# Kernel optimization log

Hardware: AMD Instinct MI355X
Metric: run time of the kernel (lower is better)

## Reference

```python
import jax, jax.numpy as jnp
import numpy as np

NUM_HEADS = 8


def setup_inputs() -> dict:
    key = jax.random.key(0)
    ks = jax.random.split(key, 5)
    b, c, h, w = 8, 256, 32, 32
    x = jax.random.normal(ks[0], (b, c, h, w), dtype=jnp.float32)
    w_qkv = jax.random.normal(ks[1], (3 * c, c), dtype=jnp.float32) * (c ** -0.5)
    b_qkv = jax.random.normal(ks[2], (3 * c,), dtype=jnp.float32) * 0.02
    w_proj = jax.random.normal(ks[3], (c, c), dtype=jnp.float32) * (c ** -0.5)
    b_proj = jax.random.normal(ks[4], (c,), dtype=jnp.float32) * 0.02
    return {"x": x, "w_qkv": w_qkv, "b_qkv": b_qkv, "w_proj": w_proj, "b_proj": b_proj}


def reference(x, w_qkv, b_qkv, w_proj, b_proj):
    b, c, h, w = x.shape
    nh = NUM_HEADS
    dh = c // nh
    L = h * w
    scale = dh ** -0.5
    # 1x1 conv == per-pixel GEMM
    qkv = jnp.einsum('bchw,oc->bohw', x, w_qkv) + b_qkv[None, :, None, None]
    qkv = qkv.reshape(b, 3, nh, dh, L)
    q, k, v = qkv[:, 0], qkv[:, 1], qkv[:, 2]  # each (b, nh, dh, L)
    attn = jnp.einsum('bhdi,bhdj->bhij', q, k) * scale  # (b, nh, L, L)
    attn = jax.nn.softmax(attn, axis=-1)
    out = jnp.einsum('bhdj,bhij->bhdi', v, attn)  # (b, nh, dh, L)
    out = out.reshape(b, c, h, w)
    proj = jnp.einsum('bchw,oc->bohw', out, w_proj) + b_proj[None, :, None, None]
    return x + proj
```

## Files before the change

kernel.cpp:

```cpp
#include <hip/hip_runtime.h>
#include <math.h>

#define B_   8
#define CIN  256
#define L_   1024
#define NH_  8
#define DH_  32

typedef __attribute__((ext_vector_type(8))) short short8;
typedef __attribute__((ext_vector_type(4))) short short4v;
typedef __attribute__((ext_vector_type(4))) float f32x4;
typedef __attribute__((ext_vector_type(4))) unsigned int uint4v;
typedef __attribute__((ext_vector_type(2))) unsigned int uint2v;

__device__ inline short f2bf_hu(float f) {
    union { float f; unsigned u; } v; v.f = f;
    return (short)((v.u + 0x8000u) >> 16);
}
__device__ inline unsigned pkbf2(float a, float b) {
    union { float f; unsigned u; } x, y; x.f = a; y.f = b;
    return __builtin_amdgcn_perm(y.u + 0x8000u, x.u + 0x8000u, 0x07060302u);
}

__global__ __launch_bounds__(256) void qkv_gemm(
    const float* __restrict__ x, const float* __restrict__ w,
    const float* __restrict__ bias, short* __restrict__ qkvT)
{
    __shared__ short Xs[64][40];
    __shared__ short Wt[128][40];
    const int t = threadIdx.x, lane = t & 63, wv = t >> 6;
    const int n = lane & 15, quad = lane >> 4;
    const int b = blockIdx.z, o0 = blockIdx.y * 128, l0 = blockIdx.x * 64;

    float bias_r[8];
    #pragma unroll
    for (int nf = 0; nf < 8; nf++) bias_r[nf] = bias[o0 + nf * 16 + n];

    f32x4 acc[8];
    #pragma unroll
    for (int nf = 0; nf < 8; nf++) acc[nf] = (f32x4){0.f, 0.f, 0.f, 0.f};

    const int cS = t >> 3, lsS = (t & 7) * 8;

    for (int c0 = 0; c0 < CIN; c0 += 32) {
        {
            const float* xp = &x[(((size_t)b * CIN + c0 + cS) << 10) + l0 + lsS];
            const float4 xa = *(const float4*)xp;
            const float4 xb = *(const float4*)(xp + 4);
            const float vals[8] = {xa.x, xa.y, xa.z, xa.w, xb.x, xb.y, xb.z, xb.w};
            #pragma unroll
            for (int k = 0; k < 8; k++) {
                const int l = lsS + k;
                const int col = (((cS >> 3) ^ (l & 3)) << 3) | (cS & 7);
                Xs[l][col] = f2bf_hu(vals[k]);
            }
        }
        {
            const int o = t >> 1, cs = (t & 1) * 16;
            const float* wp = &w[(size_t)(o0 + o) * CIN + c0 + cs];
            const float4 w0 = *(const float4*)(wp);
            const float4 w1 = *(const float4*)(wp + 4);
            const float4 w2 = *(const float4*)(wp + 8);
            const float4 w3 = *(const float4*)(wp + 12);
            uint4v pa = { pkbf2(w0.x, w0.y), pkbf2(w0.z, w0.w),
                          pkbf2(w1.x, w1.y), pkbf2(w1.z, w1.w) };
            uint4v pb = { pkbf2(w2.x, w2.y), pkbf2(w2.z, w2.w),
                          pkbf2(w3.x, w3.y), pkbf2(w3.z, w3.w) };
            *(uint4v*)&Wt[o][cs]     = pa;
            *(uint4v*)&Wt[o][cs + 8] = pb;
        }
        __syncthreads();

        const int arow = wv * 16 + n;
        const short8 af = *(const short8*)&Xs[arow][(quad ^ (arow & 3)) * 8];
        #pragma unroll
        for (int nf = 0; nf < 8; nf++) {
            const short8 bf = *(const short8*)&Wt[nf * 16 + n][quad * 8];
            acc[nf] = __builtin_amdgcn_mfma_f32_16x16x32_bf16(af, bf, acc[nf], 0, 0, 0);
        }
        __syncthreads();
    }

    #pragma unroll
    for (int reg = 0; reg < 4; reg++) {
        const size_t l = l0 + wv * 16 + quad * 4 + reg;
        short* row = qkvT + (((size_t)b << 10) + l) * 768 + o0 + n;
        #pragma unroll
        for (int nf = 0; nf < 8; nf++)
            row[nf * 16] = f2bf_hu(acc[nf][reg] + bias_r[nf]);
    }
}

__global__ __launch_bounds__(256) void proj_gemm(
    const short* __restrict__ aT, const float* __restrict__ w,
    const float* __restrict__ bias, const float* __restrict__ resid,
    float* __restrict__ out)
{
    __shared__ short Xs[64][40];
    __shared__ short Wt[64][40];
    const int t = threadIdx.x, lane = t & 63, wv = t >> 6;
    const int n = lane & 15, quad = lane >> 4;
    const int b = blockIdx.z, o0 = blockIdx.y * 64, l0 = blockIdx.x * 64;

    float bias_r[4];
    #pragma unroll
    for (int reg = 0; reg < 4; reg++) bias_r[reg] = bias[o0 + wv * 16 + quad * 4 + reg];

    f32x4 acc[4];
    #pragma unroll
    for (int nf = 0; nf < 4; nf++) acc[nf] = (f32x4){0.f, 0.f, 0.f, 0.f};

    for (int c0 = 0; c0 < CIN; c0 += 32) {
        {
            const int l = t >> 2, cs = (t & 3) * 8;
            *(uint4v*)&Xs[l][cs] =
                *(const uint4v*)&aT[(((size_t)b << 10) + l0 + l) * CIN + c0 + cs];
        }
        {
            const int o = t >> 2, cs = (t & 3) * 8;
            const float* wp = &w[(size_t)(o0 + o) * CIN + c0 + cs];
            const float4 a4 = *(const float4*)(wp);
            const float4 b4 = *(const float4*)(wp + 4);
            uint4v pw = { pkbf2(a4.x, a4.y), pkbf2(a4.z, a4.w),
                          pkbf2(b4.x, b4.y), pkbf2(b4.z, b4.w) };
            *(uint4v*)&Wt[o][cs] = pw;
        }
        __syncthreads();

        const short8 af = *(const short8*)&Wt[wv * 16 + n][quad * 8];
        #pragma unroll
        for (int nf = 0; nf < 4; nf++) {
            const short8 bf = *(const short8*)&Xs[nf * 16 + n][quad * 8];
            acc[nf] = __builtin_amdgcn_mfma_f32_16x16x32_bf16(af, bf, acc[nf], 0, 0, 0);
        }
        __syncthreads();
    }

    #pragma unroll
    for (int reg = 0; reg < 4; reg++) {
        const int o = o0 + wv * 16 + quad * 4 + reg;
        #pragma unroll
        for (int nf = 0; nf < 4; nf++) {
            const size_t off = (((size_t)b * CIN + o) << 10) + l0 + nf * 16 + n;
            out[off] = acc[nf][reg] + bias_r[reg] + resid[off];
        }
    }
}

__global__ __launch_bounds__(256) void attn_mfma(
    const short* __restrict__ qkvT, short* __restrict__ attnoT)
{
    __shared__ short Vt[2][32][80];
    __shared__ __align__(16) char umem[128 * 88 * 2];
    short (*Ss)[88] = (short(*)[88])umem;
    float (*OtT)[38] = (float(*)[38])umem;

    const int t = threadIdx.x, lane = t & 63, wv = t >> 6;
    const int n = lane & 15, quad = lane >> 4;
    const int id = blockIdx.x;
    const int bh = id & 63;
    const int b = bh >> 3, h = bh & 7;
    const int i0 = (id >> 6) * 128;

    const short* base = qkvT + ((size_t)b << 10) * 768;

    short8 qa[2];
    #pragma unroll
    for (int a = 0; a < 2; a++)
        qa[a] = *(const short8*)&base[(size_t)(i0 + wv * 32 + a * 16 + n) * 768
                                      + h * DH_ + quad * 8];

    short8 vf2;
    {
        const short one = (n == 0) ? (short)0x3F80 : (short)0;
        #pragma unroll
        for (int u = 0; u < 8; u++) vf2[u] = one;
    }

    f32x4 o_acc[2][3];
    #pragma unroll
    for (int a = 0; a < 2; a++)
        #pragma unroll
        for (int nf = 0; nf < 3; nf++) o_acc[a][nf] = (f32x4){0.f, 0.f, 0.f, 0.f};

    const float K1 = 0.25503510f;
    const float K2 = 11.54156036f;
    const int TSTRIDE = 64 * 768;

    const short* kp0 = base + 256 + h * DH_ + (size_t)n * 768 + quad * 8;
    const short* kp1 = kp0 + 16 * 768;
    const short* kp2 = kp0 + 32 * 768;
    const short* kp3 = kp0 + 48 * 768;
    const int jS = t >> 3, dsS = (t & 7) * 4;
    const short* vp0 = base + 512 + h * DH_ + (size_t)jS * 768 + dsS;
    const short* vp1 = vp0 + 32 * 768;

    const int vmsk = ((dsS >> 2) & 7) << 3;
    const int vwo0 = dsS * 80 + (jS ^ vmsk);
    const int vwo1 = dsS * 80 + ((jS + 32) ^ vmsk);
    short* const vtb0 = &Vt[0][0][0];
    short* const vtb1 = &Vt[1][0][0];
    short* const ssw  = &Ss[wv * 32 + n][quad * 4];
    const short* const ssr = &Ss[wv * 32 + n][quad * 8];
    int vro[2][2];
    #pragma unroll
    for (int nf = 0; nf < 2; nf++) {
        const int dv = nf * 16 + n;
        const int msk = ((dv >> 2) & 7) << 3;
        #pragma unroll
        for (int kk = 0; kk < 2; kk++)
            vro[kk][nf] = dv * 80 + ((kk * 32 + quad * 8) ^ msk);
    }

    short8 kfA[4], kfB[4];

    auto stageV = [&](short* vtb) {
        const short4v a = *(const short4v*)vp0; vp0 += TSTRIDE;
        const short4v c = *(const short4v*)vp1; vp1 += TSTRIDE;
        #pragma unroll
        for (int u = 0; u < 4; u++) {
            vtb[vwo0 + u * 80] = a[u];
            vtb[vwo1 + u * 80] = c[u];
        }
    };
    auto loadK = [&](short8* kf) {
        kf[0] = *(const short8*)kp0; kp0 += TSTRIDE;
        kf[1] = *(const short8*)kp1; kp1 += TSTRIDE;
        kf[2] = *(const short8*)kp2; kp2 += TSTRIDE;
        kf[3] = *(const short8*)kp3; kp3 += TSTRIDE;
    };
    auto tile = [&](const short8* kf, const short* vtb) {
        #pragma unroll
        for (int f = 0; f < 4; f++) {
            #pragma unroll
            for (int a = 0; a < 2; a++) {
                f32x4 z = {0.f, 0.f, 0.f, 0.f};
                const f32x4 sv = __builtin_amdgcn_mfma_f32_16x16x32_bf16(kf[f], qa[a], z, 0, 0, 0);
                const float p0 = __builtin_amdgcn_exp2f(fmaf(sv[0], K1, -K2));
                const float p1 = __builtin_amdgcn_exp2f(fmaf(sv[1], K1, -K2));
                const float p2 = __builtin_amdgcn_exp2f(fmaf(sv[2], K1, -K2));
                const float p3 = __builtin_amdgcn_exp2f(fmaf(sv[3], K1, -K2));
                uint2v pk = { pkbf2(p0, p1), pkbf2(p2, p3) };
                *(uint2v*)(ssw + a * 16 * 88 + f * 16) = pk;
            }
        }
        #pragma unroll
        for (int kk = 0; kk < 2; kk++) {
            short8 pf[2];
            #pragma unroll
            for (int a = 0; a < 2; a++)
                pf[a] = *(const short8*)(ssr + a * 16 * 88 + kk * 32);
            #pragma unroll
            for (int nf = 0; nf < 2; nf++) {
                const short8 vf = *(const short8*)(vtb + vro[kk][nf]);
                #pragma unroll
                for (int a = 0; a < 2; a++)
                    o_acc[a][nf] = __builtin_amdgcn_mfma_f32_16x16x32_bf16(pf[a], vf, o_acc[a][nf], 0, 0, 0);
            }
            #pragma unroll
            for (int a = 0; a < 2; a++)
                o_acc[a][2] = __builtin_amdgcn_mfma_f32_16x16x32_bf16(pf[a], vf2, o_acc[a][2], 0, 0, 0);
        }
    };

    stageV(vtb0);
    loadK(kfA);

    for (int itp = 0; itp < 8; itp++) {
        __syncthreads();
        stageV(vtb1);
        loadK(kfB);
        tile(kfA, vtb0);
        __syncthreads();
        if (itp < 7) { stageV(vtb0); loadK(kfA); }
        tile(kfB, vtb1);
    }

    __syncthreads();
    #pragma unroll
    for (int a = 0; a < 2; a++)
        #pragma unroll
        for (int r = 0; r < 4; r++) {
            const float lv  = __shfl(o_acc[a][2][r], lane & 48, 64);
            const float inv = 1.f / lv;
            const int il = wv * 32 + a * 16 + quad * 4 + r;
            OtT[il][n]      = o_acc[a][0][r] * inv;
            OtT[il][16 + n] = o_acc[a][1][r] * inv;
        }
    __syncthreads();
    short* ob = attnoT + (((size_t)b << 10) + i0) * CIN + h * DH_;
    #pragma unroll
    for (int r = 0; r < 4; r++) {
        const int idx = t + r * 256;
        const int l = idx >> 3, cs = (idx & 7) * 4;
        uint2v pv;
        pv.x = pkbf2(OtT[l][cs],     OtT[l][cs + 1]);
        pv.y = pkbf2(OtT[l][cs + 2], OtT[l][cs + 3]);
        *(uint2v*)&ob[(size_t)l * CIN + cs] = pv;
    }
}

extern "C" void kernel_launch(void* const* d_in, const int* in_sizes, int n_in,
                              void* d_out, int out_size, void* d_ws, size_t ws_size,
                              hipStream_t stream) {
    const float* x      = (const float*)d_in[0];
    const float* w_qkv  = (const float*)d_in[1];
    const float* b_qkv  = (const float*)d_in[2];
    const float* w_proj = (const float*)d_in[3];
    const float* b_proj = (const float*)d_in[4];
    float* out = (float*)d_out;

    short* qkvT   = (short*)d_ws;
    short* attnoT = qkvT + (size_t)B_ * L_ * 768;

    qkv_gemm<<<dim3(16, 6, B_), 256, 0, stream>>>(x, w_qkv, b_qkv, qkvT);
    attn_mfma<<<dim3(512), 256, 0, stream>>>(qkvT, attnoT);
    proj_gemm<<<dim3(16, 4, B_), 256, 0, stream>>>(attnoT, w_proj, b_proj, x, out);
}
```

Before: 115.7 us.

## Store V transposed from QKV GEMM so attention reads V fragments directly from global

The QKV GEMM now writes Q and K into a token-major buffer and V into a separate channel-major (d, L) buffer. The attention kernel can then load V MFMA operands straight from global memory into registers, the same way it loads K. This removes the shared-memory V staging, its swizzled scatter writes, and both __syncthreads per iteration. In exchange, the GEMM's V epilogue does strided scalar stores, and the attention kernel relies on cache and register prefetch rather than LDS reuse for V.

```diff
diff --git a/kernel.cpp b/kernel.cpp
--- a/kernel.cpp
+++ b/kernel.cpp
@@ -24,7 +24,8 @@
 
 __global__ __launch_bounds__(256) void qkv_gemm(
     const float* __restrict__ x, const float* __restrict__ w,
-    const float* __restrict__ bias, short* __restrict__ qkvT)
+    const float* __restrict__ bias, short* __restrict__ qkT,
+    short* __restrict__ vT)
 {
     __shared__ short Xs[64][40];
     __shared__ short Wt[128][40];
@@ -81,13 +82,26 @@
         __syncthreads();
     }
 
-    #pragma unroll
-    for (int reg = 0; reg < 4; reg++) {
-        const size_t l = l0 + wv * 16 + quad * 4 + reg;
-        short* row = qkvT + (((size_t)b << 10) + l) * 768 + o0 + n;
-        #pragma unroll
-        for (int nf = 0; nf < 8; nf++)
-            row[nf * 16] = f2bf_hu(acc[nf][reg] + bias_r[nf]);
+    if (o0 < 512) {
+        #pragma unroll
+        for (int reg = 0; reg < 4; reg++) {
+            const size_t l = l0 + wv * 16 + quad * 4 + reg;
+            short* row = qkT + ((((size_t)b << 10) + l) << 9) + o0 + n;
+            #pragma unroll
+            for (int nf = 0; nf < 8; nf++)
+                row[nf * 16] = f2bf_hu(acc[nf][reg] + bias_r[nf]);
+        }
+    } else {
+        #pragma unroll
+        for (int reg = 0; reg < 4; reg++) {
+            const size_t l = l0 + wv * 16 + quad * 4 + reg;
+            #pragma unroll
+            for (int nf = 0; nf < 8; nf++) {
+                const int ov = o0 - 512 + nf * 16 + n;
+                vT[(((size_t)b << 8) + ov << 10) + l] =
+                    f2bf_hu(acc[nf][reg] + bias_r[nf]);
+            }
+        }
     }
 }
 
@@ -148,9 +162,9 @@
 }
 
 __global__ __launch_bounds__(256) void attn_mfma(
-    const short* __restrict__ qkvT, short* __restrict__ attnoT)
+    const short* __restrict__ qkT, const short* __restrict__ vT,
+    short* __restrict__ attnoT)
 {
-    __shared__ short Vt[2][32][80];
     __shared__ __align__(16) char umem[128 * 88 * 2];
     short (*Ss)[88] = (short(*)[88])umem;
     float (*OtT)[38] = (float(*)[38])umem;
@@ -162,13 +176,14 @@
     const int b = bh >> 3, h = bh & 7;
     const int i0 = (id >> 6) * 128;
 
-    const short* base = qkvT + ((size_t)b << 10) * 768;
+    const short* qbase = qkT + ((size_t)b << 19) + h * DH_;
+    const short* kbase = qbase + 256;
+    const short* vtb   = vT + ((size_t)((b << 3) + h) << 15);
 
     short8 qa[2];
     #pragma unroll
     for (int a = 0; a < 2; a++)
-        qa[a] = *(const short8*)&base[(size_t)(i0 + wv * 32 + a * 16 + n) * 768
-                                      + h * DH_ + quad * 8];
+        qa[a] = *(const short8*)&qbase[(size_t)(i0 + wv * 32 + a * 16 + n) * 512 + quad * 8];
 
     short8 vf2;
     {
@@ -185,51 +200,34 @@
 
     const float K1 = 0.25503510f;
     const float K2 = 11.54156036f;
-    const int TSTRIDE = 64 * 768;
-
-    const short* kp0 = base + 256 + h * DH_ + (size_t)n * 768 + quad * 8;
-    const short* kp1 = kp0 + 16 * 768;
-    const short* kp2 = kp0 + 32 * 768;
-    const short* kp3 = kp0 + 48 * 768;
-    const int jS = t >> 3, dsS = (t & 7) * 4;
-    const short* vp0 = base + 512 + h * DH_ + (size_t)jS * 768 + dsS;
-    const short* vp1 = vp0 + 32 * 768;
-
-    const int vmsk = ((dsS >> 2) & 7) << 3;
-    const int vwo0 = dsS * 80 + (jS ^ vmsk);
-    const int vwo1 = dsS * 80 + ((jS + 32) ^ vmsk);
-    short* const vtb0 = &Vt[0][0][0];
-    short* const vtb1 = &Vt[1][0][0];
+    const int KSTRIDE = 64 * 512;
+    const int VSTRIDE = 64;
+
+    const short* kp0 = kbase + (size_t)n * 512 + quad * 8;
+    const short* kp1 = kp0 + 16 * 512;
+    const short* kp2 = kp0 + 32 * 512;
+    const short* kp3 = kp0 + 48 * 512;
+    const short* vp00 = vtb + ((size_t)n) * 1024 + quad * 8;
+    const short* vp01 = vp00 + 16 * 1024;
+    const short* vp10 = vp00 + 32;
+    const short* vp11 = vp01 + 32;
+
     short* const ssw  = &Ss[wv * 32 + n][quad * 4];
     const short* const ssr = &Ss[wv * 32 + n][quad * 8];
-    int vro[2][2];
-    #pragma unroll
-    for (int nf = 0; nf < 2; nf++) {
-        const int dv = nf * 16 + n;
-        const int msk = ((dv >> 2) & 7) << 3;
-        #pragma unroll
-        for (int kk = 0; kk < 2; kk++)
-            vro[kk][nf] = dv * 80 + ((kk * 32 + quad * 8) ^ msk);
-    }
-
-    short8 kfA[4], kfB[4];
-
-    auto stageV = [&](short* vtb) {
-        const short4v a = *(const short4v*)vp0; vp0 += TSTRIDE;
-        const short4v c = *(const short4v*)vp1; vp1 += TSTRIDE;
-        #pragma unroll
-        for (int u = 0; u < 4; u++) {
-            vtb[vwo0 + u * 80] = a[u];
-            vtb[vwo1 + u * 80] = c[u];
-        }
+
+    short8 kfA[4], vfA[2][2], kfB[4], vfB[2][2];
+
+    auto loadKV = [&](short8* kf, short8 vf[2][2]) {
+        kf[0] = *(const short8*)kp0; kp0 += KSTRIDE;
+        kf[1] = *(const short8*)kp1; kp1 += KSTRIDE;
+        kf[2] = *(const short8*)kp2; kp2 += KSTRIDE;
+        kf[3] = *(const short8*)kp3; kp3 += KSTRIDE;
+        vf[0][0] = *(const short8*)vp00; vp00 += VSTRIDE;
+        vf[0][1] = *(const short8*)vp01; vp01 += VSTRIDE;
+        vf[1][0] = *(const short8*)vp10; vp10 += VSTRIDE;
+        vf[1][1] = *(const short8*)vp11; vp11 += VSTRIDE;
     };
-    auto loadK = [&](short8* kf) {
-        kf[0] = *(const short8*)kp0; kp0 += TSTRIDE;
-        kf[1] = *(const short8*)kp1; kp1 += TSTRIDE;
-        kf[2] = *(const short8*)kp2; kp2 += TSTRIDE;
-        kf[3] = *(const short8*)kp3; kp3 += TSTRIDE;
-    };
-    auto tile = [&](const short8* kf, const short* vtb) {
+    auto tile = [&](const short8* kf, const short8 vf[2][2]) {
         #pragma unroll
         for (int f = 0; f < 4; f++) {
             #pragma unroll
@@ -251,29 +249,22 @@
             for (int a = 0; a < 2; a++)
                 pf[a] = *(const short8*)(ssr + a * 16 * 88 + kk * 32);
             #pragma unroll
-            for (int nf = 0; nf < 2; nf++) {
-                const short8 vf = *(const short8*)(vtb + vro[kk][nf]);
+            for (int nf = 0; nf < 2; nf++)
                 #pragma unroll
                 for (int a = 0; a < 2; a++)
-                    o_acc[a][nf] = __builtin_amdgcn_mfma_f32_16x16x32_bf16(pf[a], vf, o_acc[a][nf], 0, 0, 0);
-            }
+                    o_acc[a][nf] = __builtin_amdgcn_mfma_f32_16x16x32_bf16(pf[a], vf[kk][nf], o_acc[a][nf], 0, 0, 0);
             #pragma unroll
             for (int a = 0; a < 2; a++)
                 o_acc[a][2] = __builtin_amdgcn_mfma_f32_16x16x32_bf16(pf[a], vf2, o_acc[a][2], 0, 0, 0);
         }
     };
 
-    stageV(vtb0);
-    loadK(kfA);
-
+    loadKV(kfA, vfA);
     for (int itp = 0; itp < 8; itp++) {
-        __syncthreads();
-        stageV(vtb1);
-        loadK(kfB);
-        tile(kfA, vtb0);
-        __syncthreads();
-        if (itp < 7) { stageV(vtb0); loadK(kfA); }
-        tile(kfB, vtb1);
+        loadKV(kfB, vfB);
+        tile(kfA, vfA);
+        if (itp < 7) loadKV(kfA, vfA);
+        tile(kfB, vfB);
     }
 
     __syncthreads();
@@ -310,10 +301,11 @@
     const float* b_proj = (const float*)d_in[4];
     float* out = (float*)d_out;
 
-    short* qkvT   = (short*)d_ws;
-    short* attnoT = qkvT + (size_t)B_ * L_ * 768;
-
-    qkv_gemm<<<dim3(16, 6, B_), 256, 0, stream>>>(x, w_qkv, b_qkv, qkvT);
-    attn_mfma<<<dim3(512), 256, 0, stream>>>(qkvT, attnoT);
+    short* qkT    = (short*)d_ws;
+    short* vT     = qkT + (size_t)B_ * L_ * 512;
+    short* attnoT = vT  + (size_t)B_ * CIN * L_;
+
+    qkv_gemm<<<dim3(16, 6, B_), 256, 0, stream>>>(x, w_qkv, b_qkv, qkT, vT);
+    attn_mfma<<<dim3(512), 256, 0, stream>>>(qkT, vT, attnoT);
     proj_gemm<<<dim3(16, 4, B_), 256, 0, stream>>>(attnoT, w_proj, b_proj, x, out);
 }
```

New measurement: 126.3 us. 1.09x slower.

## Retile QKV GEMM to 128x96 blocks with packed bf16 X staging

Applied to the files above, without the earlier changes.

The QKV projection GEMM moves from 64(L)x128(O) tiles to 128(L)x96(O) tiles, so each wave computes two 16-row A fragments that share every B fragment load. The X tile load is reorganised so each thread reads 4 channels x 4 pixels and writes packed bf16 pairs to shared memory, replacing 8 scalar 16-bit stores. Together these aim to cut LDS traffic and store instructions per MFMA, with the grid changing from 16x6 to 8x8 blocks per batch. In exchange, a quarter of threads sit idle during the weight load and each thread holds more accumulator registers.

```diff
diff --git a/kernel.cpp b/kernel.cpp
--- a/kernel.cpp
+++ b/kernel.cpp
@@ -26,36 +26,43 @@
     const float* __restrict__ x, const float* __restrict__ w,
     const float* __restrict__ bias, short* __restrict__ qkvT)
 {
-    __shared__ short Xs[64][40];
-    __shared__ short Wt[128][40];
+    __shared__ short Xs[128][40];
+    __shared__ short Wt[96][40];
     const int t = threadIdx.x, lane = t & 63, wv = t >> 6;
     const int n = lane & 15, quad = lane >> 4;
-    const int b = blockIdx.z, o0 = blockIdx.y * 128, l0 = blockIdx.x * 64;
-
-    float bias_r[8];
-    #pragma unroll
-    for (int nf = 0; nf < 8; nf++) bias_r[nf] = bias[o0 + nf * 16 + n];
-
-    f32x4 acc[8];
-    #pragma unroll
-    for (int nf = 0; nf < 8; nf++) acc[nf] = (f32x4){0.f, 0.f, 0.f, 0.f};
-
-    const int cS = t >> 3, lsS = (t & 7) * 8;
+    const int b = blockIdx.z, o0 = blockIdx.y * 96, l0 = blockIdx.x * 128;
+
+    float bias_r[6];
+    #pragma unroll
+    for (int nf = 0; nf < 6; nf++) bias_r[nf] = bias[o0 + nf * 16 + n];
+
+    f32x4 acc[2][6];
+    #pragma unroll
+    for (int a = 0; a < 2; a++)
+        #pragma unroll
+        for (int nf = 0; nf < 6; nf++) acc[a][nf] = (f32x4){0.f, 0.f, 0.f, 0.f};
+
+    const int cS4 = (t & 7) * 4;
+    const int lg4 = (t >> 3) * 4;
 
     for (int c0 = 0; c0 < CIN; c0 += 32) {
         {
-            const float* xp = &x[(((size_t)b * CIN + c0 + cS) << 10) + l0 + lsS];
-            const float4 xa = *(const float4*)xp;
-            const float4 xb = *(const float4*)(xp + 4);
-            const float vals[8] = {xa.x, xa.y, xa.z, xa.w, xb.x, xb.y, xb.z, xb.w};
-            #pragma unroll
-            for (int k = 0; k < 8; k++) {
-                const int l = lsS + k;
-                const int col = (((cS >> 3) ^ (l & 3)) << 3) | (cS & 7);
-                Xs[l][col] = f2bf_hu(vals[k]);
+            const float* xp = &x[(((size_t)b * CIN + c0 + cS4) << 10) + l0 + lg4];
+            float xv[4][4];
+            #pragma unroll
+            for (int cr = 0; cr < 4; cr++) {
+                const float4 v = *(const float4*)(xp + ((size_t)cr << 10));
+                xv[cr][0] = v.x; xv[cr][1] = v.y; xv[cr][2] = v.z; xv[cr][3] = v.w;
             }
-        }
-        {
+            #pragma unroll
+            for (int r = 0; r < 4; r++) {
+                const int l = lg4 + r;
+                const int col = (((cS4 >> 3) ^ (l & 3)) << 3) | (cS4 & 7);
+                uint2v pk = { pkbf2(xv[0][r], xv[1][r]), pkbf2(xv[2][r], xv[3][r]) };
+                *(uint2v*)&Xs[l][col] = pk;
+            }
+        }
+        if (t < 192) {
             const int o = t >> 1, cs = (t & 1) * 16;
             const float* wp = &w[(size_t)(o0 + o) * CIN + c0 + cs];
             const float4 w0 = *(const float4*)(wp);
@@ -71,24 +78,30 @@
         }
         __syncthreads();
 
-        const int arow = wv * 16 + n;
-        const short8 af = *(const short8*)&Xs[arow][(quad ^ (arow & 3)) * 8];
-        #pragma unroll
-        for (int nf = 0; nf < 8; nf++) {
+        const int gsw = (quad ^ (n & 3)) * 8;
+        short8 af[2];
+        af[0] = *(const short8*)&Xs[wv * 32 + n][gsw];
+        af[1] = *(const short8*)&Xs[wv * 32 + 16 + n][gsw];
+        #pragma unroll
+        for (int nf = 0; nf < 6; nf++) {
             const short8 bf = *(const short8*)&Wt[nf * 16 + n][quad * 8];
-            acc[nf] = __builtin_amdgcn_mfma_f32_16x16x32_bf16(af, bf, acc[nf], 0, 0, 0);
-        }
-        __syncthreads();
-    }
-
-    #pragma unroll
-    for (int reg = 0; reg < 4; reg++) {
-        const size_t l = l0 + wv * 16 + quad * 4 + reg;
-        short* row = qkvT + (((size_t)b << 10) + l) * 768 + o0 + n;
-        #pragma unroll
-        for (int nf = 0; nf < 8; nf++)
-            row[nf * 16] = f2bf_hu(acc[nf][reg] + bias_r[nf]);
-    }
+            #pragma unroll
+            for (int a = 0; a < 2; a++)
+                acc[a][nf] = __builtin_amdgcn_mfma_f32_16x16x32_bf16(af[a], bf, acc[a][nf], 0, 0, 0);
+        }
+        __syncthreads();
+    }
+
+    #pragma unroll
+    for (int a = 0; a < 2; a++)
+        #pragma unroll
+        for (int reg = 0; reg < 4; reg++) {
+            const size_t l = l0 + wv * 32 + a * 16 + quad * 4 + reg;
+            short* row = qkvT + (((size_t)b << 10) + l) * 768 + o0 + n;
+            #pragma unroll
+            for (int nf = 0; nf < 6; nf++)
+                row[nf * 16] = f2bf_hu(acc[a][nf][reg] + bias_r[nf]);
+        }
 }
 
 __global__ __launch_bounds__(256) void proj_gemm(
@@ -313,7 +326,7 @@
     short* qkvT   = (short*)d_ws;
     short* attnoT = qkvT + (size_t)B_ * L_ * 768;
 
-    qkv_gemm<<<dim3(16, 6, B_), 256, 0, stream>>>(x, w_qkv, b_qkv, qkvT);
+    qkv_gemm<<<dim3(8, 8, B_), 256, 0, stream>>>(x, w_qkv, b_qkv, qkvT);
     attn_mfma<<<dim3(512), 256, 0, stream>>>(qkvT, attnoT);
     proj_gemm<<<dim3(16, 4, B_), 256, 0, stream>>>(attnoT, w_proj, b_proj, x, out);
 }
```

Result: slower. 118.8 us (+2.7%).

## Split attention over two key halves and merge partials in projection GEMM

Applied to the files above, without the earlier changes.

The attention kernel now splits the key/value range into two halves, launching twice as many blocks. Each block writes unnormalised fp32 partial outputs and partial softmax denominators to workspace. The projection GEMM sums the two partials, divides by the combined denominator and converts to bf16 while staging its input tile. The aim is more blocks per CU for better latency hiding and load balance, at the cost of extra fp32 workspace traffic (partials are written and read back) and a small amount of added arithmetic in the projection load path.

```diff
diff --git a/kernel.cpp b/kernel.cpp
--- a/kernel.cpp
+++ b/kernel.cpp
@@ -92,9 +92,9 @@
 }
 
 __global__ __launch_bounds__(256) void proj_gemm(
-    const short* __restrict__ aT, const float* __restrict__ w,
-    const float* __restrict__ bias, const float* __restrict__ resid,
-    float* __restrict__ out)
+    const float* __restrict__ partO, const float* __restrict__ partD,
+    const float* __restrict__ w, const float* __restrict__ bias,
+    const float* __restrict__ resid, float* __restrict__ out)
 {
     __shared__ short Xs[64][40];
     __shared__ short Wt[64][40];
@@ -113,8 +113,22 @@
     for (int c0 = 0; c0 < CIN; c0 += 32) {
         {
             const int l = t >> 2, cs = (t & 3) * 8;
-            *(uint4v*)&Xs[l][cs] =
-                *(const uint4v*)&aT[(((size_t)b << 10) + l0 + l) * CIN + c0 + cs];
+            const int h = c0 >> 5;
+            const size_t li = ((size_t)b << 10) + l0 + l;
+            const float* p0 = &partO[(0 * (size_t)B_ * L_ + li) * CIN + c0 + cs];
+            const float* p1 = &partO[(1 * (size_t)B_ * L_ + li) * CIN + c0 + cs];
+            const float d = partD[(0 * (size_t)B_ * L_ + li) * NH_ + h]
+                          + partD[(1 * (size_t)B_ * L_ + li) * NH_ + h];
+            const float inv = 1.f / d;
+            const float4 a0 = *(const float4*)p0;
+            const float4 a1 = *(const float4*)(p0 + 4);
+            const float4 b0 = *(const float4*)p1;
+            const float4 b1 = *(const float4*)(p1 + 4);
+            uint4v pw = { pkbf2((a0.x + b0.x) * inv, (a0.y + b0.y) * inv),
+                          pkbf2((a0.z + b0.z) * inv, (a0.w + b0.w) * inv),
+                          pkbf2((a1.x + b1.x) * inv, (a1.y + b1.y) * inv),
+                          pkbf2((a1.z + b1.z) * inv, (a1.w + b1.w) * inv) };
+            *(uint4v*)&Xs[l][cs] = pw;
         }
         {
             const int o = t >> 2, cs = (t & 3) * 8;
@@ -148,19 +162,19 @@
 }
 
 __global__ __launch_bounds__(256) void attn_mfma(
-    const short* __restrict__ qkvT, short* __restrict__ attnoT)
+    const short* __restrict__ qkvT, float* __restrict__ partO,
+    float* __restrict__ partD)
 {
     __shared__ short Vt[2][32][80];
-    __shared__ __align__(16) char umem[128 * 88 * 2];
-    short (*Ss)[88] = (short(*)[88])umem;
-    float (*OtT)[38] = (float(*)[38])umem;
+    __shared__ __align__(16) short Ss[128][88];
 
     const int t = threadIdx.x, lane = t & 63, wv = t >> 6;
     const int n = lane & 15, quad = lane >> 4;
     const int id = blockIdx.x;
     const int bh = id & 63;
     const int b = bh >> 3, h = bh & 7;
-    const int i0 = (id >> 6) * 128;
+    const int i0 = ((id >> 6) & 7) * 128;
+    const int s  = id >> 9;
 
     const short* base = qkvT + ((size_t)b << 10) * 768;
 
@@ -187,12 +201,13 @@
     const float K2 = 11.54156036f;
     const int TSTRIDE = 64 * 768;
 
-    const short* kp0 = base + 256 + h * DH_ + (size_t)n * 768 + quad * 8;
+    const size_t soff = (size_t)s * 8 * TSTRIDE;
+    const short* kp0 = base + 256 + h * DH_ + (size_t)n * 768 + quad * 8 + soff;
     const short* kp1 = kp0 + 16 * 768;
     const short* kp2 = kp0 + 32 * 768;
     const short* kp3 = kp0 + 48 * 768;
     const int jS = t >> 3, dsS = (t & 7) * 4;
-    const short* vp0 = base + 512 + h * DH_ + (size_t)jS * 768 + dsS;
+    const short* vp0 = base + 512 + h * DH_ + (size_t)jS * 768 + dsS + soff;
     const short* vp1 = vp0 + 32 * 768;
 
     const int vmsk = ((dsS >> 2) & 7) << 3;
@@ -266,37 +281,34 @@
     stageV(vtb0);
     loadK(kfA);
 
-    for (int itp = 0; itp < 8; itp++) {
+    for (int itp = 0; itp < 4; itp++) {
         __syncthreads();
         stageV(vtb1);
         loadK(kfB);
         tile(kfA, vtb0);
         __syncthreads();
-        if (itp < 7) { stageV(vtb0); loadK(kfA); }
+        if (itp < 3) { stageV(vtb0); loadK(kfA); }
         tile(kfB, vtb1);
     }
 
-    __syncthreads();
-    #pragma unroll
-    for (int a = 0; a < 2; a++)
+    #pragma unroll
+    for (int a = 0; a < 2; a++) {
         #pragma unroll
         for (int r = 0; r < 4; r++) {
-            const float lv  = __shfl(o_acc[a][2][r], lane & 48, 64);
-            const float inv = 1.f / lv;
-            const int il = wv * 32 + a * 16 + quad * 4 + r;
-            OtT[il][n]      = o_acc[a][0][r] * inv;
-            OtT[il][16 + n] = o_acc[a][1][r] * inv;
-        }
-    __syncthreads();
-    short* ob = attnoT + (((size_t)b << 10) + i0) * CIN + h * DH_;
-    #pragma unroll
-    for (int r = 0; r < 4; r++) {
-        const int idx = t + r * 256;
-        const int l = idx >> 3, cs = (idx & 7) * 4;
-        uint2v pv;
-        pv.x = pkbf2(OtT[l][cs],     OtT[l][cs + 1]);
-        pv.y = pkbf2(OtT[l][cs + 2], OtT[l][cs + 3]);
-        *(uint2v*)&ob[(size_t)l * CIN + cs] = pv;
+            const int il = i0 + wv * 32 + a * 16 + quad * 4 + r;
+            float* po = partO + (((size_t)s * B_ + b) * L_ + il) * CIN + h * DH_;
+            po[n]      = o_acc[a][0][r];
+            po[16 + n] = o_acc[a][1][r];
+        }
+    }
+    if (n == 0) {
+        #pragma unroll
+        for (int a = 0; a < 2; a++)
+            #pragma unroll
+            for (int r = 0; r < 4; r++) {
+                const int il = i0 + wv * 32 + a * 16 + quad * 4 + r;
+                partD[(((size_t)s * B_ + b) * L_ + il) * NH_ + h] = o_acc[a][2][r];
+            }
     }
 }
 
@@ -310,10 +322,11 @@
     const float* b_proj = (const float*)d_in[4];
     float* out = (float*)d_out;
 
-    short* qkvT   = (short*)d_ws;
-    short* attnoT = qkvT + (size_t)B_ * L_ * 768;
+    short* qkvT  = (short*)d_ws;
+    float* partO = (float*)(qkvT + (size_t)B_ * L_ * 768);
+    float* partD = partO + (size_t)2 * B_ * L_ * CIN;
 
     qkv_gemm<<<dim3(16, 6, B_), 256, 0, stream>>>(x, w_qkv, b_qkv, qkvT);
-    attn_mfma<<<dim3(512), 256, 0, stream>>>(qkvT, attnoT);
-    proj_gemm<<<dim3(16, 4, B_), 256, 0, stream>>>(attnoT, w_proj, b_proj, x, out);
-}
+    attn_mfma<<<dim3(1024), 256, 0, stream>>>(qkvT, partO, partD);
+    proj_gemm<<<dim3(16, 4, B_), 256, 0, stream>>>(partO, partD, w_proj, b_proj, x, out);
+}
```

Result: no change. 114.9 us (-0.7%).
